# Optimization experiments

Measured on AMD Instinct MI355X. Metric: run time of the kernel, lower is better.

## Reference

```python
import jax, jax.numpy as jnp
import numpy as np

NUM_NODES = 16384
NUM_EDGES = 524288
D_IN = 128
D_OUT = 128


def setup_inputs() -> dict:
    key = jax.random.key(0)
    k1, k2, k3 = jax.random.split(key, 3)
    x = jax.random.normal(k1, (NUM_NODES, D_IN), dtype=jnp.float32)
    edge_index = jax.random.randint(k2, (2, NUM_EDGES), 0, NUM_NODES, dtype=jnp.int64)
    # Xavier-uniform-like W; B is zeros in the original init but we use small
    # random values so its branch contributes to the output numerically.
    limit = float(np.sqrt(6.0 / (D_IN + D_OUT)))
    W = jax.random.uniform(k3, (D_OUT, D_IN), dtype=jnp.float32, minval=-limit, maxval=limit)
    B = jax.random.normal(jax.random.fold_in(key, 7), (D_OUT, D_IN), dtype=jnp.float32) * 0.02
    return {"x": x, "edge_index": edge_index, "W": W, "B": B}


def reference(x, edge_index, W, B):
    n = x.shape[0]
    src = edge_index[0]
    dst = edge_index[1]
    # Dense adjacency: A[i, j] = 1 iff edge j -> i (duplicates collapse via set)
    A = jnp.zeros((n, n), dtype=x.dtype).at[dst, src].set(1.0)
    deg = A.sum(axis=1)                      # in-degree per node
    d_inv = 1.0 / jnp.maximum(deg, 1.0)      # clamp(min=1)
    agg = d_inv[:, None] * (A @ x)           # D_inv @ A @ x (diag as row scale)
    out = agg @ W.T + x @ B.T                # F.linear(.., W) + F.linear(x, B)
    return out
```

## Files before the change

kernel.cpp:

```cpp
#include <hip/hip_runtime.h>

#define NN  16384
#define NE  524288
#define D   128
#define GEMMB 512
#define FILLB 256

#define OFF_BM 0u
#define OFF_Y  33554432u
#define OFF_Z  41943040u
#define BM_BYTES 33554432u

typedef __bf16 bf16x4 __attribute__((ext_vector_type(4)));
typedef __bf16 bf16x8 __attribute__((ext_vector_type(8)));
typedef float  f32x4  __attribute__((ext_vector_type(4)));
typedef unsigned short u16;

__global__ __launch_bounds__(256, 2) void k1(const float* __restrict__ x,
                                             const int* __restrict__ ei,
                                             const float* __restrict__ W,
                                             const float* __restrict__ Bm,
                                             float* __restrict__ y,
                                             float* __restrict__ z,
                                             unsigned* __restrict__ bm) {
  __shared__ __bf16 sA[32][40];
  __shared__ __bf16 sB[256][40];
  __shared__ int s_any;
  int b = blockIdx.x, t = threadIdx.x;

  if (b < GEMMB) {
    int l = t & 63, wid = t >> 6;
    int g = l >> 4, ln = l & 15;
    int mh = wid & 1, nh = wid >> 1;
    int row0 = b * 32;
    f32x4 acc[8];
#pragma unroll
    for (int nb = 0; nb < 8; ++nb) acc[nb] = f32x4{0.f, 0.f, 0.f, 0.f};

    for (int kc = 0; kc < 4; ++kc) {
      int kb = kc * 32;
      __syncthreads();
      {
        int rr = t >> 3, q = t & 7;
        float4 v = *(const float4*)&x[(size_t)(row0 + rr) * D + kb + q * 4];
        bf16x4 w = {(__bf16)v.x, (__bf16)v.y, (__bf16)v.z, (__bf16)v.w};
        *(bf16x4*)&sA[rr][q * 4] = w;
      }
#pragma unroll
      for (int u = 0; u < 8; ++u) {
        int f = u * 256 + t;
        int rr = f >> 3, q = f & 7;
        const float* Bp = (rr < 128) ? &W[(size_t)rr * D] : &Bm[(size_t)(rr - 128) * D];
        float4 v = *(const float4*)&Bp[kb + q * 4];
        bf16x4 w = {(__bf16)v.x, (__bf16)v.y, (__bf16)v.z, (__bf16)v.w};
        *(bf16x4*)&sB[rr][q * 4] = w;
      }
      __syncthreads();
      bf16x8 afr = *(const bf16x8*)&sA[mh * 16 + ln][g * 8];
#pragma unroll
      for (int nb = 0; nb < 8; ++nb) {
        bf16x8 bfr = *(const bf16x8*)&sB[nh * 128 + nb * 16 + ln][g * 8];
        acc[nb] = __builtin_amdgcn_mfma_f32_16x16x32_bf16(afr, bfr, acc[nb], 0, 0, 0);
      }
    }
    float* dstm = (nh == 0) ? y : z;
#pragma unroll
    for (int nb = 0; nb < 8; ++nb)
#pragma unroll
      for (int i = 0; i < 4; ++i)
        dstm[(size_t)(row0 + mh * 16 + g * 4 + i) * D + nb * 16 + ln] = acc[nb][i];
  } else {
    if (t == 0) s_any = 0;
    __syncthreads();
    int base = (b - GEMMB) * 2048;
    int any = 0;
#pragma unroll
    for (int u = 0; u < 8; ++u) any |= ei[2 * (base + u * 256 + t) + 1];
    if (any) atomicOr(&s_any, 1);
    __syncthreads();
    int is32 = s_any;
#pragma unroll
    for (int u = 0; u < 8; ++u) {
      int i = base + u * 256 + t;
      int s = is32 ? ei[i] : ei[2 * i];
      int d = is32 ? ei[NE + i] : ei[2 * (NE + i)];
      atomicOr(&bm[((size_t)d << 9) + (s >> 5)], 1u << (s & 31));
    }
  }
}

#define RPB 8
__global__ __launch_bounds__(256) void gather_k(const unsigned* __restrict__ bm,
                                                const float* __restrict__ y,
                                                const float* __restrict__ z,
                                                float* __restrict__ out) {
  __shared__ u16 s_col[RPB][128];
  int t = threadIdx.x, lane = t & 31, r = t >> 5;
  int row = blockIdx.x * RPB + r;
  const unsigned* bmr = bm + ((size_t)row << 9);

  int base = 0;
  for (int ch = 0; ch < 16; ++ch) {
    int w = ch * 32 + lane;
    unsigned m = bmr[w];
    int c = __popc(m);
    int inc = c;
#pragma unroll
    for (int dlt = 1; dlt < 32; dlt <<= 1) {
      int n = __shfl_up(inc, dlt, 32);
      if (lane >= dlt) inc += n;
    }
    int p = base + inc - c;
    while (m) {
      int bpos = __ffs(m) - 1;
      m &= m - 1;
      if (p < 128) s_col[r][p] = (u16)(w * 32 + bpos);
      ++p;
    }
    base += __shfl(inc, 31, 32);
  }
  int deg = base;
  int k = deg > 128 ? 128 : deg;
  float dinv = 1.0f / (float)(deg > 0 ? deg : 1);

  float4 a[8];
#pragma unroll
  for (int u = 0; u < 8; ++u) a[u] = float4{0.f, 0.f, 0.f, 0.f};
  const float* yl = y + lane * 4;
#define FMA4(aa, vv) { aa.x += vv.x; aa.y += vv.y; aa.z += vv.z; aa.w += vv.w; }
  int j = 0;
  for (; j + 8 <= k; j += 8) {
    float4 v[8];
#pragma unroll
    for (int u = 0; u < 8; ++u)
      v[u] = *(const float4*)(yl + (size_t)s_col[r][j + u] * D);
#pragma unroll
    for (int u = 0; u < 8; ++u) FMA4(a[u], v[u])
  }
  for (; j < k; ++j) {
    float4 v0 = *(const float4*)(yl + (size_t)s_col[r][j] * D);
    FMA4(a[0], v0)
  }
#undef FMA4
#pragma unroll
  for (int u = 4; u < 8; ++u) {
    a[u - 4].x += a[u].x; a[u - 4].y += a[u].y;
    a[u - 4].z += a[u].z; a[u - 4].w += a[u].w;
  }
  float4 zv = *(const float4*)(z + (size_t)row * D + lane * 4);
  float4 o;
  o.x = (a[0].x + a[1].x + a[2].x + a[3].x) * dinv + zv.x;
  o.y = (a[0].y + a[1].y + a[2].y + a[3].y) * dinv + zv.y;
  o.z = (a[0].z + a[1].z + a[2].z + a[3].z) * dinv + zv.z;
  o.w = (a[0].w + a[1].w + a[2].w + a[3].w) * dinv + zv.w;
  *(float4*)(out + (size_t)row * D + lane * 4) = o;
}

extern "C" void kernel_launch(void* const* d_in, const int* in_sizes, int n_in,
                              void* d_out, int out_size, void* d_ws, size_t ws_size,
                              hipStream_t stream) {
  const float* x = (const float*)d_in[0];
  const int* ei = (const int*)d_in[1];
  const float* W = (const float*)d_in[2];
  const float* Bm = (const float*)d_in[3];
  float* out = (float*)d_out;
  char* ws = (char*)d_ws;
  unsigned* bm = (unsigned*)(ws + OFF_BM);
  float* y = (float*)(ws + OFF_Y);
  float* z = (float*)(ws + OFF_Z);

  hipMemsetAsync(bm, 0, BM_BYTES, stream);
  k1<<<GEMMB + FILLB, 256, 0, stream>>>(x, ei, W, Bm, y, z, bm);
  gather_k<<<NN / RPB, 256, 0, stream>>>(bm, y, z, out);
}
```

Baseline: 70.64 us.

## Build per-row neighbor lists during bitmap fill instead of rescanning the bitmap

The fill stage now uses the old value returned by atomicOr to spot first-time edges. For each one it bumps a per-destination counter and writes the source index into a 128-slot slab. The gather kernel then reads just the count and the compact slab, so it no longer scans the 2KB bitmap row per node with popcount and prefix scans, which removes about 32MB of bitmap reads. hipMemsetAsync is replaced by a custom zeroing kernel that clears both the bitmap and the counters. The cost is a second atomic per unique edge, and neighbor order becomes nondeterministic, so floating-point summation order can vary between runs.

```diff
diff --git a/kernel.cpp b/kernel.cpp
--- a/kernel.cpp
+++ b/kernel.cpp
@@ -6,15 +6,24 @@
 #define GEMMB 512
 #define FILLB 256
 
-#define OFF_BM 0u
-#define OFF_Y  33554432u
-#define OFF_Z  41943040u
-#define BM_BYTES 33554432u
+#define OFF_BM   0u
+#define OFF_CNT  33554432u
+#define OFF_SLAB 33619968u
+#define OFF_Y    37814272u
+#define OFF_Z    46202880u
+#define NZ4      2101248u
 
 typedef __bf16 bf16x4 __attribute__((ext_vector_type(4)));
 typedef __bf16 bf16x8 __attribute__((ext_vector_type(8)));
 typedef float  f32x4  __attribute__((ext_vector_type(4)));
 typedef unsigned short u16;
+
+__global__ __launch_bounds__(256) void zero_k(uint4* __restrict__ p) {
+  int i = blockIdx.x * 256 + threadIdx.x;
+#pragma unroll
+  for (int u = 0; u < 16; ++u)
+    p[(size_t)u * 131328 + i] = uint4{0, 0, 0, 0};
+}
 
 __global__ __launch_bounds__(256, 2) void k1(const float* __restrict__ x,
                                              const int* __restrict__ ei,
@@ -22,7 +31,9 @@
                                              const float* __restrict__ Bm,
                                              float* __restrict__ y,
                                              float* __restrict__ z,
-                                             unsigned* __restrict__ bm) {
+                                             unsigned* __restrict__ bm,
+                                             int* __restrict__ cnt,
+                                             u16* __restrict__ slab) {
   __shared__ __bf16 sA[32][40];
   __shared__ __bf16 sB[256][40];
   __shared__ int s_any;
@@ -84,44 +95,30 @@
       int i = base + u * 256 + t;
       int s = is32 ? ei[i] : ei[2 * i];
       int d = is32 ? ei[NE + i] : ei[2 * (NE + i)];
-      atomicOr(&bm[((size_t)d << 9) + (s >> 5)], 1u << (s & 31));
+      unsigned bit = 1u << (s & 31);
+      unsigned old = atomicOr(&bm[((size_t)d << 9) + (s >> 5)], bit);
+      if (!(old & bit)) {
+        int slot = atomicAdd(&cnt[d], 1);
+        if (slot < 128) slab[((size_t)d << 7) + slot] = (u16)s;
+      }
     }
   }
 }
 
 #define RPB 8
-__global__ __launch_bounds__(256) void gather_k(const unsigned* __restrict__ bm,
+__global__ __launch_bounds__(256) void gather_k(const int* __restrict__ cnt,
+                                                const u16* __restrict__ slab,
                                                 const float* __restrict__ y,
                                                 const float* __restrict__ z,
                                                 float* __restrict__ out) {
   __shared__ u16 s_col[RPB][128];
   int t = threadIdx.x, lane = t & 31, r = t >> 5;
   int row = blockIdx.x * RPB + r;
-  const unsigned* bmr = bm + ((size_t)row << 9);
-
-  int base = 0;
-  for (int ch = 0; ch < 16; ++ch) {
-    int w = ch * 32 + lane;
-    unsigned m = bmr[w];
-    int c = __popc(m);
-    int inc = c;
-#pragma unroll
-    for (int dlt = 1; dlt < 32; dlt <<= 1) {
-      int n = __shfl_up(inc, dlt, 32);
-      if (lane >= dlt) inc += n;
-    }
-    int p = base + inc - c;
-    while (m) {
-      int bpos = __ffs(m) - 1;
-      m &= m - 1;
-      if (p < 128) s_col[r][p] = (u16)(w * 32 + bpos);
-      ++p;
-    }
-    base += __shfl(inc, 31, 32);
-  }
-  int deg = base;
-  int k = deg > 128 ? 128 : deg;
-  float dinv = 1.0f / (float)(deg > 0 ? deg : 1);
+  int k = cnt[row];
+  if (k > 128) k = 128;
+  const u16* srow = slab + ((size_t)row << 7);
+  for (int j = lane; j < k; j += 32) s_col[r][j] = srow[j];
+  float dinv = 1.0f / (float)(k > 0 ? k : 1);
 
   float4 a[8];
 #pragma unroll
@@ -166,10 +163,12 @@
   float* out = (float*)d_out;
   char* ws = (char*)d_ws;
   unsigned* bm = (unsigned*)(ws + OFF_BM);
+  int* cnt = (int*)(ws + OFF_CNT);
+  u16* slab = (u16*)(ws + OFF_SLAB);
   float* y = (float*)(ws + OFF_Y);
   float* z = (float*)(ws + OFF_Z);
 
-  hipMemsetAsync(bm, 0, BM_BYTES, stream);
-  k1<<<GEMMB + FILLB, 256, 0, stream>>>(x, ei, W, Bm, y, z, bm);
-  gather_k<<<NN / RPB, 256, 0, stream>>>(bm, y, z, out);
+  zero_k<<<513, 256, 0, stream>>>((uint4*)ws);
+  k1<<<GEMMB + FILLB, 256, 0, stream>>>(x, ei, W, Bm, y, z, bm, cnt, slab);
+  gather_k<<<NN / RPB, 256, 0, stream>>>(cnt, slab, y, z, out);
 }
```

Measured after the change: 99.42 us. +40.8%, slower.
